# Kernel optimization log

Measured on AMD Instinct MI355X. Metric: run time of the kernel, lower is better.

Reference implementation:

```python
import jax, jax.numpy as jnp
import numpy as np

M_SIGMA = 1.0 * 0.997 / 3.0  # args.m * 0.997 / 3


def setup_inputs() -> dict:
    key = jax.random.key(0)
    k1, k2 = jax.random.split(key)
    B, D = 64, 512        # batch (sketches+shapes), embedding dim
    P = 256               # points per cloud
    embeddings = jax.random.normal(k1, (B, D), dtype=jnp.float32)
    xyz = jax.random.normal(k2, (B, P, 3), dtype=jnp.float32)
    return {"embeddings": embeddings, "xyz": xyz}


def _chamfer_all_pairs(shapes):
    # shapes: [M, P, 3]. Returns cd[i, j] = chamfer(shapes[i], shapes[j]),
    # chamfer = mean_p min_q ||x_p - y_q||^2 + mean_q min_p ||x_p - y_q||^2
    sq = jnp.sum(shapes * shapes, axis=-1)                  # [M, P]
    inner = jnp.einsum('ipd,jqd->ijpq', shapes, shapes)     # [M, M, P, P]
    d2 = sq[:, None, :, None] + sq[None, :, None, :] - 2.0 * inner
    cd = jnp.min(d2, axis=3).mean(axis=2) + jnp.min(d2, axis=2).mean(axis=2)
    return cd  # [M, M]


def reference(embeddings, xyz):
    # L2-normalize embeddings along feature dim
    emb = embeddings / jnp.linalg.norm(embeddings, axis=1, keepdims=True)
    B = emb.shape[0]
    mb = B // 2
    shapes = xyz[mb:]                                       # [mb, P, 3]
    sketch_feat, shape_feat = emb[:mb], emb[mb:]            # [mb, D] each
    inner_dot = sketch_feat @ shape_feat.T                  # [mb, mb]
    cd = _chamfer_all_pairs(shapes)                         # [mb, mb]
    real_dist = (cd ** 2) / (2.0 * M_SIGMA ** 2)
    p = jax.nn.softmax(-real_dist, axis=1)
    p_hat = jax.nn.softmax(inner_dot, axis=1)               # use_softmax=True
    reg = jnp.mean(jnp.abs(p_hat - p))                      # use_KL=False
    return reg
```

## Files before the change

### kernel.cpp

```cpp
#include <hip/hip_runtime.h>
#include <math.h>


typedef float f32x2 __attribute__((ext_vector_type(2)));

__device__ __forceinline__ float waveReduceSum64(float v) {
    #pragma unroll
    for (int m = 32; m > 0; m >>= 1) v += __shfl_xor(v, m, 64);
    return v;
}

__global__ __launch_bounds__(256) void pairs_kernel(const float* __restrict__ emb,
                                                    const float* __restrict__ xyz,
                                                    float* __restrict__ cdHalf,
                                                    float* __restrict__ dots) {
    const int t = threadIdx.x;
    const int b = blockIdx.x;

    __shared__ __align__(16) float S[3 * 256];
    __shared__ float red[4];
    float* Sx = S;
    float* Sy = S + 256;
    float* Sz = S + 512;

    if (b < 992) {
        const int pb  = b >> 1;
        const int dir = b & 1;
        int i = 0, rem = pb;
        while (rem >= (31 - i)) { rem -= (31 - i); ++i; }
        const int j = i + 1 + rem;

        const int outer = dir ? j : i;
        const int inner = dir ? i : j;

        const float* Po = xyz + (32 + outer) * 768;
        const float* Pi = xyz + (32 + inner) * 768;

        const float ix = Pi[3*t], iy = Pi[3*t+1], iz = Pi[3*t+2];
        Sx[t] = ix; Sy[t] = iy; Sz[t] = iz;
        const float px = Po[3*t], py = Po[3*t+1], pz = Po[3*t+2];
        __syncthreads();

        const f32x2 Px = {px, px}, Py = {py, py}, Pz = {pz, pz};
        f32x2 m0 = {3.4e38f, 3.4e38f}, m1 = {3.4e38f, 3.4e38f};

        #pragma unroll 4
        for (int s = 0; s < 256; s += 4) {
            const float4 vx = *(const float4*)&Sx[s];
            const float4 vy = *(const float4*)&Sy[s];
            const float4 vz = *(const float4*)&Sz[s];
            {
                const f32x2 bx = {vx.x, vx.y}, by = {vy.x, vy.y}, bz = {vz.x, vz.y};
                f32x2 dx = Px - bx, dy = Py - by, dz = Pz - bz;
                f32x2 d = dx*dx + dy*dy + dz*dz;
                m0.x = fminf(m0.x, d.x); m0.y = fminf(m0.y, d.y);
            }
            {
                const f32x2 bx = {vx.z, vx.w}, by = {vy.z, vy.w}, bz = {vz.z, vz.w};
                f32x2 dx = Px - bx, dy = Py - by, dz = Pz - bz;
                f32x2 d = dx*dx + dy*dy + dz*dz;
                m1.x = fminf(m1.x, d.x); m1.y = fminf(m1.y, d.y);
            }
        }
        const float mn = fminf(fminf(m0.x, m0.y), fminf(m1.x, m1.y));

        float v = waveReduceSum64(mn);
        if ((t & 63) == 0) red[t >> 6] = v;
        __syncthreads();
        if (t == 0)
            cdHalf[b] = (red[0] + red[1] + red[2] + red[3]) * (1.0f / 256.0f);
    } else {
        const int i = b - 992;
        float* rowi = S;
        const float* Ei = emb + i * 512;
        rowi[t]       = Ei[t];
        rowi[t + 256] = Ei[t + 256];
        __syncthreads();

        const int w    = t >> 6;
        const int lane = t & 63;

        float ni = 0.0f;
        #pragma unroll
        for (int m = 0; m < 8; ++m) { float a = rowi[lane + 64*m]; ni += a*a; }
        ni = waveReduceSum64(ni);

        for (int j = w; j < 32; j += 4) {
            const float* Ej = emb + (32 + j) * 512;
            float dot = 0.0f, nj = 0.0f;
            #pragma unroll
            for (int m = 0; m < 8; ++m) {
                float a  = rowi[lane + 64*m];
                float bv = Ej[lane + 64*m];
                dot += a * bv;
                nj  += bv * bv;
            }
            dot = waveReduceSum64(dot);
            nj  = waveReduceSum64(nj);
            if (lane == 0) dots[i * 32 + j] = dot * rsqrtf(ni * nj);
        }
    }
}

__global__ __launch_bounds__(1024) void finish_kernel(const float* __restrict__ cdHalf,
                                                      const float* __restrict__ dots,
                                                      float* __restrict__ out) {
    const int t = threadIdx.x;
    const int i = t >> 5;
    const int j = t & 31;
    const float inv_denom = 1.0f / (2.0f * (0.997f / 3.0f) * (0.997f / 3.0f));

    float c;
    if (i == j) {
        c = 0.0f;
    } else {
        const int a  = min(i, j), bb = max(i, j);
        const int pb = a * 31 - (a * (a - 1)) / 2 + (bb - a - 1);
        c = cdHalf[2 * pb] + cdHalf[2 * pb + 1];
    }
    float s = -(c * c) * inv_denom;
    float h = dots[t];

    float m1 = s;
    #pragma unroll
    for (int k = 16; k > 0; k >>= 1) m1 = fmaxf(m1, __shfl_xor(m1, k, 32));
    float e1 = expf(s - m1);
    float sum1 = e1;
    #pragma unroll
    for (int k = 16; k > 0; k >>= 1) sum1 += __shfl_xor(sum1, k, 32);
    float p = e1 / sum1;

    float m2 = h;
    #pragma unroll
    for (int k = 16; k > 0; k >>= 1) m2 = fmaxf(m2, __shfl_xor(m2, k, 32));
    float e2 = expf(h - m2);
    float sum2 = e2;
    #pragma unroll
    for (int k = 16; k > 0; k >>= 1) sum2 += __shfl_xor(sum2, k, 32);
    float ph = e2 / sum2;

    float a = fabsf(ph - p);
    a = waveReduceSum64(a);

    __shared__ float red[16];
    if ((t & 63) == 0) red[t >> 6] = a;
    __syncthreads();
    if (t == 0) {
        float tot = 0.0f;
        #pragma unroll
        for (int k = 0; k < 16; ++k) tot += red[k];
        out[0] = tot * (1.0f / 1024.0f);
    }
}

extern "C" void kernel_launch(void* const* d_in, const int* in_sizes, int n_in,
                              void* d_out, int out_size, void* d_ws, size_t ws_size,
                              hipStream_t stream) {
    const float* emb = (const float*)d_in[0];
    const float* xyz = (const float*)d_in[1];
    float* cdHalf = (float*)d_ws;
    float* dots   = cdHalf + 1024;
    float* out    = (float*)d_out;

    hipLaunchKernelGGL(pairs_kernel, dim3(1024), dim3(256), 0, stream, emb, xyz, cdHalf, dots);
    hipLaunchKernelGGL(finish_kernel, dim3(1), dim3(1024), 0, stream, cdHalf, dots, out);
}
```

Before: 66.22 us.

## Stage one cloud in LDS per block and test two query clouds against it

```diff
diff --git a/kernel.cpp b/kernel.cpp
--- a/kernel.cpp
+++ b/kernel.cpp
@@ -16,63 +16,75 @@
                                                     float* __restrict__ dots) {
     const int t = threadIdx.x;
     const int b = blockIdx.x;
+    const int c = b >> 4;
+    const int g = b & 15;
 
     __shared__ __align__(16) float S[3 * 256];
-    __shared__ float red[4];
+    __shared__ float red0[4], red1[4];
     float* Sx = S;
     float* Sy = S + 256;
     float* Sz = S + 512;
 
-    if (b < 992) {
-        const int pb  = b >> 1;
-        const int dir = b & 1;
-        int i = 0, rem = pb;
-        while (rem >= (31 - i)) { rem -= (31 - i); ++i; }
-        const int j = i + 1 + rem;
+    const int k0 = 2 * g;
+    const bool hasO1 = (g < 15);
+    const int o0 = k0 + (k0 >= c ? 1 : 0);
+    const int k1 = k0 + 1;
+    const int o1 = hasO1 ? (k1 + (k1 >= c ? 1 : 0)) : o0;
 
-        const int outer = dir ? j : i;
-        const int inner = dir ? i : j;
+    const float* Pc = xyz + (32 + c) * 768;
+    const float* P0 = xyz + (32 + o0) * 768;
+    const float* P1 = xyz + (32 + o1) * 768;
 
-        const float* Po = xyz + (32 + outer) * 768;
-        const float* Pi = xyz + (32 + inner) * 768;
+    Sx[t] = Pc[3*t]; Sy[t] = Pc[3*t+1]; Sz[t] = Pc[3*t+2];
+    const float p0x = P0[3*t], p0y = P0[3*t+1], p0z = P0[3*t+2];
+    const float p1x = P1[3*t], p1y = P1[3*t+1], p1z = P1[3*t+2];
+    __syncthreads();
 
-        const float ix = Pi[3*t], iy = Pi[3*t+1], iz = Pi[3*t+2];
-        Sx[t] = ix; Sy[t] = iy; Sz[t] = iz;
-        const float px = Po[3*t], py = Po[3*t+1], pz = Po[3*t+2];
-        __syncthreads();
+    const f32x2 Ax = {p0x, p0x}, Ay = {p0y, p0y}, Az = {p0z, p0z};
+    const f32x2 Bx = {p1x, p1x}, By = {p1y, p1y}, Bz = {p1z, p1z};
 
-        const f32x2 Px = {px, px}, Py = {py, py}, Pz = {pz, pz};
-        f32x2 m0 = {3.4e38f, 3.4e38f}, m1 = {3.4e38f, 3.4e38f};
+    float accA = 3.4e38f, accB = 3.4e38f;
 
-        #pragma unroll 4
-        for (int s = 0; s < 256; s += 4) {
-            const float4 vx = *(const float4*)&Sx[s];
-            const float4 vy = *(const float4*)&Sy[s];
-            const float4 vz = *(const float4*)&Sz[s];
-            {
-                const f32x2 bx = {vx.x, vx.y}, by = {vy.x, vy.y}, bz = {vz.x, vz.y};
-                f32x2 dx = Px - bx, dy = Py - by, dz = Pz - bz;
-                f32x2 d = dx*dx + dy*dy + dz*dz;
-                m0.x = fminf(m0.x, d.x); m0.y = fminf(m0.y, d.y);
-            }
-            {
-                const f32x2 bx = {vx.z, vx.w}, by = {vy.z, vy.w}, bz = {vz.z, vz.w};
-                f32x2 dx = Px - bx, dy = Py - by, dz = Pz - bz;
-                f32x2 d = dx*dx + dy*dy + dz*dz;
-                m1.x = fminf(m1.x, d.x); m1.y = fminf(m1.y, d.y);
-            }
+    #pragma unroll 4
+    for (int s = 0; s < 256; s += 4) {
+        const float4 vx = *(const float4*)&Sx[s];
+        const float4 vy = *(const float4*)&Sy[s];
+        const float4 vz = *(const float4*)&Sz[s];
+        {
+            const f32x2 qx = {vx.x, vx.y}, qy = {vy.x, vy.y}, qz = {vz.x, vz.y};
+            f32x2 dx = Ax - qx, dy = Ay - qy, dz = Az - qz;
+            f32x2 d = dx*dx + dy*dy + dz*dz;
+            accA = fminf(accA, fminf(d.x, d.y));
+            f32x2 ex = Bx - qx, ey = By - qy, ez = Bz - qz;
+            f32x2 e = ex*ex + ey*ey + ez*ez;
+            accB = fminf(accB, fminf(e.x, e.y));
         }
-        const float mn = fminf(fminf(m0.x, m0.y), fminf(m1.x, m1.y));
+        {
+            const f32x2 qx = {vx.z, vx.w}, qy = {vy.z, vy.w}, qz = {vz.z, vz.w};
+            f32x2 dx = Ax - qx, dy = Ay - qy, dz = Az - qz;
+            f32x2 d = dx*dx + dy*dy + dz*dz;
+            accA = fminf(accA, fminf(d.x, d.y));
+            f32x2 ex = Bx - qx, ey = By - qy, ez = Bz - qz;
+            f32x2 e = ex*ex + ey*ey + ez*ez;
+            accB = fminf(accB, fminf(e.x, e.y));
+        }
+    }
 
-        float v = waveReduceSum64(mn);
-        if ((t & 63) == 0) red[t >> 6] = v;
-        __syncthreads();
-        if (t == 0)
-            cdHalf[b] = (red[0] + red[1] + red[2] + red[3]) * (1.0f / 256.0f);
-    } else {
-        const int i = b - 992;
+    float v0 = waveReduceSum64(accA);
+    float v1 = waveReduceSum64(accB);
+    if ((t & 63) == 0) { red0[t >> 6] = v0; red1[t >> 6] = v1; }
+    __syncthreads();
+    if (t == 0) {
+        cdHalf[c * 32 + o0] = (red0[0] + red0[1] + red0[2] + red0[3]) * (1.0f / 256.0f);
+        if (hasO1)
+            cdHalf[c * 32 + o1] = (red1[0] + red1[1] + red1[2] + red1[3]) * (1.0f / 256.0f);
+    }
+
+    if (!hasO1) {
+        const int i = c;
         float* rowi = S;
         const float* Ei = emb + i * 512;
+        __syncthreads();
         rowi[t]       = Ei[t];
         rowi[t + 256] = Ei[t + 256];
         __syncthreads();
@@ -110,14 +122,7 @@
     const int j = t & 31;
     const float inv_denom = 1.0f / (2.0f * (0.997f / 3.0f) * (0.997f / 3.0f));
 
-    float c;
-    if (i == j) {
-        c = 0.0f;
-    } else {
-        const int a  = min(i, j), bb = max(i, j);
-        const int pb = a * 31 - (a * (a - 1)) / 2 + (bb - a - 1);
-        c = cdHalf[2 * pb] + cdHalf[2 * pb + 1];
-    }
+    float c = (i == j) ? 0.0f : (cdHalf[j * 32 + i] + cdHalf[i * 32 + j]);
     float s = -(c * c) * inv_denom;
     float h = dots[t];
 
@@ -162,6 +167,6 @@
     float* dots   = cdHalf + 1024;
     float* out    = (float*)d_out;
 
-    hipLaunchKernelGGL(pairs_kernel, dim3(1024), dim3(256), 0, stream, emb, xyz, cdHalf, dots);
+    hipLaunchKernelGGL(pairs_kernel, dim3(512), dim3(256), 0, stream, emb, xyz, cdHalf, dots);
     hipLaunchKernelGGL(finish_kernel, dim3(1), dim3(1024), 0, stream, cdHalf, dots, out);
 }
```

New measurement: 72.29 us. 9.2% more time.

## Fuse finish kernel into pairs kernel via last-block atomic counter

Applied to the files above, without the earlier changes.

```diff
diff --git a/kernel.cpp b/kernel.cpp
--- a/kernel.cpp
+++ b/kernel.cpp
@@ -10,15 +10,18 @@
     return v;
 }
 
-__global__ __launch_bounds__(256) void pairs_kernel(const float* __restrict__ emb,
+__global__ __launch_bounds__(256) void fused_kernel(const float* __restrict__ emb,
                                                     const float* __restrict__ xyz,
                                                     float* __restrict__ cdHalf,
-                                                    float* __restrict__ dots) {
+                                                    float* __restrict__ dots,
+                                                    unsigned int* __restrict__ ctr,
+                                                    float* __restrict__ out) {
     const int t = threadIdx.x;
     const int b = blockIdx.x;
 
     __shared__ __align__(16) float S[3 * 256];
     __shared__ float red[4];
+    __shared__ int lastFlag;
     float* Sx = S;
     float* Sy = S + 256;
     float* Sz = S + 512;
@@ -42,7 +45,7 @@
         __syncthreads();
 
         const f32x2 Px = {px, px}, Py = {py, py}, Pz = {pz, pz};
-        f32x2 m0 = {3.4e38f, 3.4e38f}, m1 = {3.4e38f, 3.4e38f};
+        float m0 = 3.4e38f;
 
         #pragma unroll 4
         for (int s = 0; s < 256; s += 4) {
@@ -53,18 +56,17 @@
                 const f32x2 bx = {vx.x, vx.y}, by = {vy.x, vy.y}, bz = {vz.x, vz.y};
                 f32x2 dx = Px - bx, dy = Py - by, dz = Pz - bz;
                 f32x2 d = dx*dx + dy*dy + dz*dz;
-                m0.x = fminf(m0.x, d.x); m0.y = fminf(m0.y, d.y);
+                m0 = fminf(m0, fminf(d.x, d.y));
             }
             {
                 const f32x2 bx = {vx.z, vx.w}, by = {vy.z, vy.w}, bz = {vz.z, vz.w};
                 f32x2 dx = Px - bx, dy = Py - by, dz = Pz - bz;
                 f32x2 d = dx*dx + dy*dy + dz*dz;
-                m1.x = fminf(m1.x, d.x); m1.y = fminf(m1.y, d.y);
+                m0 = fminf(m0, fminf(d.x, d.y));
             }
         }
-        const float mn = fminf(fminf(m0.x, m0.y), fminf(m1.x, m1.y));
 
-        float v = waveReduceSum64(mn);
+        float v = waveReduceSum64(m0);
         if ((t & 63) == 0) red[t >> 6] = v;
         __syncthreads();
         if (t == 0)
@@ -100,57 +102,67 @@
             if (lane == 0) dots[i * 32 + j] = dot * rsqrtf(ni * nj);
         }
     }
-}
 
-__global__ __launch_bounds__(1024) void finish_kernel(const float* __restrict__ cdHalf,
-                                                      const float* __restrict__ dots,
-                                                      float* __restrict__ out) {
-    const int t = threadIdx.x;
-    const int i = t >> 5;
-    const int j = t & 31;
-    const float inv_denom = 1.0f / (2.0f * (0.997f / 3.0f) * (0.997f / 3.0f));
-
-    float c;
-    if (i == j) {
-        c = 0.0f;
-    } else {
-        const int a  = min(i, j), bb = max(i, j);
-        const int pb = a * 31 - (a * (a - 1)) / 2 + (bb - a - 1);
-        c = cdHalf[2 * pb] + cdHalf[2 * pb + 1];
-    }
-    float s = -(c * c) * inv_denom;
-    float h = dots[t];
-
-    float m1 = s;
-    #pragma unroll
-    for (int k = 16; k > 0; k >>= 1) m1 = fmaxf(m1, __shfl_xor(m1, k, 32));
-    float e1 = expf(s - m1);
-    float sum1 = e1;
-    #pragma unroll
-    for (int k = 16; k > 0; k >>= 1) sum1 += __shfl_xor(sum1, k, 32);
-    float p = e1 / sum1;
-
-    float m2 = h;
-    #pragma unroll
-    for (int k = 16; k > 0; k >>= 1) m2 = fmaxf(m2, __shfl_xor(m2, k, 32));
-    float e2 = expf(h - m2);
-    float sum2 = e2;
-    #pragma unroll
-    for (int k = 16; k > 0; k >>= 1) sum2 += __shfl_xor(sum2, k, 32);
-    float ph = e2 / sum2;
-
-    float a = fabsf(ph - p);
-    a = waveReduceSum64(a);
-
-    __shared__ float red[16];
-    if ((t & 63) == 0) red[t >> 6] = a;
     __syncthreads();
     if (t == 0) {
-        float tot = 0.0f;
+        __threadfence();
+        unsigned int old = atomicAdd(ctr, 1u);
+        lastFlag = (old == 1023u);
+    }
+    __syncthreads();
+    if (!lastFlag) return;
+
+    __threadfence();
+
+    const float inv_denom = 1.0f / (2.0f * (0.997f / 3.0f) * (0.997f / 3.0f));
+    float acc = 0.0f;
+
+    #pragma unroll
+    for (int r = 0; r < 4; ++r) {
+        const int idx = r * 256 + t;
+        const int i = idx >> 5;
+        const int j = idx & 31;
+
+        float c;
+        if (i == j) {
+            c = 0.0f;
+        } else {
+            const int a  = min(i, j), bb = max(i, j);
+            const int pb = a * 31 - (a * (a - 1)) / 2 + (bb - a - 1);
+            float h0 = __hip_atomic_load(&cdHalf[2 * pb],     __ATOMIC_ACQUIRE, __HIP_MEMORY_SCOPE_AGENT);
+            float h1 = __hip_atomic_load(&cdHalf[2 * pb + 1], __ATOMIC_ACQUIRE, __HIP_MEMORY_SCOPE_AGENT);
+            c = h0 + h1;
+        }
+        float s = -(c * c) * inv_denom;
+        float h = __hip_atomic_load(&dots[idx], __ATOMIC_ACQUIRE, __HIP_MEMORY_SCOPE_AGENT);
+
+        float m1 = s;
         #pragma unroll
-        for (int k = 0; k < 16; ++k) tot += red[k];
-        out[0] = tot * (1.0f / 1024.0f);
+        for (int k = 16; k > 0; k >>= 1) m1 = fmaxf(m1, __shfl_xor(m1, k, 32));
+        float e1 = expf(s - m1);
+        float sum1 = e1;
+        #pragma unroll
+        for (int k = 16; k > 0; k >>= 1) sum1 += __shfl_xor(sum1, k, 32);
+        float p = e1 / sum1;
+
+        float m2 = h;
+        #pragma unroll
+        for (int k = 16; k > 0; k >>= 1) m2 = fmaxf(m2, __shfl_xor(m2, k, 32));
+        float e2 = expf(h - m2);
+        float sum2 = e2;
+        #pragma unroll
+        for (int k = 16; k > 0; k >>= 1) sum2 += __shfl_xor(sum2, k, 32);
+        float ph = e2 / sum2;
+
+        acc += fabsf(ph - p);
     }
+
+    acc = waveReduceSum64(acc);
+    __syncthreads();
+    if ((t & 63) == 0) red[t >> 6] = acc;
+    __syncthreads();
+    if (t == 0)
+        out[0] = (red[0] + red[1] + red[2] + red[3]) * (1.0f / 1024.0f);
 }
 
 extern "C" void kernel_launch(void* const* d_in, const int* in_sizes, int n_in,
@@ -160,8 +172,10 @@
     const float* xyz = (const float*)d_in[1];
     float* cdHalf = (float*)d_ws;
     float* dots   = cdHalf + 1024;
+    unsigned int* ctr = (unsigned int*)((char*)d_ws + 8192);
     float* out    = (float*)d_out;
 
-    hipLaunchKernelGGL(pairs_kernel, dim3(1024), dim3(256), 0, stream, emb, xyz, cdHalf, dots);
-    hipLaunchKernelGGL(finish_kernel, dim3(1), dim3(1024), 0, stream, cdHalf, dots, out);
+    hipMemsetAsync(ctr, 0, sizeof(unsigned int), stream);
+    hipLaunchKernelGGL(fused_kernel, dim3(1024), dim3(256), 0, stream,
+                       emb, xyz, cdHalf, dots, ctr, out);
 }
```

New measurement: 85.43 us. 29.0% more time.
